# Kernel tuning notes

Hardware: AMD Instinct MI355X
Metric: run time of the kernel (lower is better)

## Reference

```python
import jax, jax.numpy as jnp
import numpy as np

D_MODEL = 1024
N_HEADS = 16
D_K = 64
D_FF = 4096
B = 8
S = 1024
NEG = -1e32
EPS = 1e-5


def _layer_norm(x, g, b):
    mu = jnp.mean(x, axis=-1, keepdims=True)
    var = jnp.var(x, axis=-1, keepdims=True)
    return (x - mu) * jax.lax.rsqrt(var + EPS) * g + b


def setup_inputs() -> dict:
    key = jax.random.key(0)
    ks = jax.random.split(key, 16)
    sc = 0.02
    inp = {
        'x': jax.random.normal(ks[0], (B, S, D_MODEL), dtype=jnp.float32),
        'Wq': jax.random.normal(ks[1], (D_MODEL, D_MODEL), jnp.float32) * sc,
        'bq': jnp.zeros((D_MODEL,), jnp.float32),
        'Wk': jax.random.normal(ks[2], (D_MODEL, D_MODEL), jnp.float32) * sc,
        'bk': jnp.zeros((D_MODEL,), jnp.float32),
        'Wv': jax.random.normal(ks[3], (D_MODEL, D_MODEL), jnp.float32) * sc,
        'bv': jnp.zeros((D_MODEL,), jnp.float32),
        'Wo': jax.random.normal(ks[4], (D_MODEL, D_MODEL), jnp.float32) * sc,
        'bo': jnp.zeros((D_MODEL,), jnp.float32),
        'W1': jax.random.normal(ks[5], (D_MODEL, D_FF), jnp.float32) * sc,
        'b1': jnp.zeros((D_FF,), jnp.float32),
        'W2': jax.random.normal(ks[6], (D_FF, D_MODEL), jnp.float32) * sc,
        'b2': jnp.zeros((D_MODEL,), jnp.float32),
        'g1': jnp.ones((D_MODEL,), jnp.float32),
        'beta1': jnp.zeros((D_MODEL,), jnp.float32),
        'g3': jnp.ones((D_MODEL,), jnp.float32),
        'beta3': jnp.zeros((D_MODEL,), jnp.float32),
    }
    return inp


def _block(x, Wq, bq, Wk, bk, Wv, bv, Wo, bo, W1, b1, W2, b2, g1, beta1, g3, beta3):
    bs, seqlen, _ = x.shape
    # QKV projections -> [b, h, s, d_k]
    def split_heads(t):
        return t.reshape(bs, seqlen, N_HEADS, D_K).transpose(0, 2, 1, 3)
    q = split_heads(x @ Wq + bq)
    k = split_heads(x @ Wk + bk)
    v = split_heads(x @ Wv + bv)
    # scores [b,h,s,s]
    scores = jnp.einsum('bhqd,bhkd->bhqk', q, k) / jnp.sqrt(jnp.float32(D_K))
    # mask=0 case: src_mask = (triu(ones, k=0) == 0) -> allow strictly lower (j < i)
    i = jnp.arange(seqlen)[:, None]
    j = jnp.arange(seqlen)[None, :]
    allowed = (j < i)  # [s, s]
    scores = jnp.where(allowed[None, None], scores, NEG)
    attn = jax.nn.softmax(scores, axis=-1)
    # zero_pad: zero out the first query row of attention probs
    attn = attn * (i > 0).astype(attn.dtype)[None, None]
    ctx = jnp.einsum('bhqk,bhkd->bhqd', attn, v)  # [b,h,s,d_k]
    concat = ctx.transpose(0, 2, 1, 3).reshape(bs, seqlen, D_MODEL)
    attn_out = concat @ Wo + bo
    # residual + LN (dropout p=0)
    h1 = _layer_norm(x + attn_out, g1, beta1)
    # position-wise FFN
    ffn = jax.nn.relu(h1 @ W1 + b1) @ W2 + b2
    out = _layer_norm(h1 + ffn, g3, beta3)
    return out


def reference(x, Wq, bq, Wk, bk, Wv, bv, Wo, bo, W1, b1, W2, b2, g1, beta1, g3, beta3):
    return _block(x, Wq, bq, Wk, bk, Wv, bv, Wo, bo, W1, b1, W2, b2, g1, beta1, g3, beta3)
```

## Files before the change

kernel.cpp:

```cpp
#include <hip/hip_runtime.h>
#include <hip/hip_bf16.h>

typedef __bf16 bf16x8 __attribute__((ext_vector_type(8)));
typedef __bf16 bf16x4 __attribute__((ext_vector_type(4)));
typedef float f32x4 __attribute__((ext_vector_type(4)));

#define GLOBAL_LOAD_LDS16(gp, lp)                                              \
  __builtin_amdgcn_global_load_lds(                                            \
      (const __attribute__((address_space(1))) void*)(gp),                     \
      (__attribute__((address_space(3))) void*)(lp), 16, 0, 0)

__global__ __launch_bounds__(256) void transpose4_f2b_k(
    const float* __restrict__ s0, const float* __restrict__ s1,
    const float* __restrict__ s2, const float* __restrict__ s3,
    __bf16* __restrict__ dst) {
  __shared__ float tile[32][33];
  const float* srcs[4] = {s0, s1, s2, s3};
  const float* src = srcs[blockIdx.z];
  __bf16* d = dst + ((size_t)blockIdx.z << 20);
  const int bx = blockIdx.x * 32, by = blockIdx.y * 32;
  const int tx = threadIdx.x & 31, ty = threadIdx.x >> 5;
#pragma unroll
  for (int i = 0; i < 32; i += 8)
    tile[ty + i][tx] = src[(size_t)(by + ty + i) * 1024 + bx + tx];
  __syncthreads();
#pragma unroll
  for (int i = 0; i < 32; i += 8)
    d[(size_t)(bx + ty + i) * 1024 + by + tx] = (__bf16)tile[tx][ty + i];
}

__global__ __launch_bounds__(256) void transpose_f2b_k(
    const float* __restrict__ src, __bf16* __restrict__ dst, int R, int C) {
  __shared__ float tile[32][33];
  const int bx = blockIdx.x * 32, by = blockIdx.y * 32;
  const int tx = threadIdx.x & 31, ty = threadIdx.x >> 5;
#pragma unroll
  for (int i = 0; i < 32; i += 8)
    tile[ty + i][tx] = src[(size_t)(by + ty + i) * C + bx + tx];
  __syncthreads();
#pragma unroll
  for (int i = 0; i < 32; i += 8)
    dst[(size_t)(bx + ty + i) * R + by + tx] = (__bf16)tile[tx][ty + i];
}

__global__ __launch_bounds__(256) void transpose_v_k(
    const __bf16* __restrict__ src, __bf16* __restrict__ dst) {
  __shared__ __bf16 tile[32][33];
  const int bh = blockIdx.z;
  const int s0 = blockIdx.x * 32, d0 = blockIdx.y * 32;
  const size_t base = (size_t)bh << 16;
  const int tx = threadIdx.x & 31, ty = threadIdx.x >> 5;
#pragma unroll
  for (int i = 0; i < 32; i += 8)
    tile[ty + i][tx] = src[base + (size_t)(s0 + ty + i) * 64 + d0 + tx];
  __syncthreads();
#pragma unroll
  for (int i = 0; i < 32; i += 8)
    dst[base + (size_t)(d0 + ty + i) * 1024 + s0 + tx] = tile[tx][ty + i];
}

__global__ __launch_bounds__(256) void convert_f2b_k(const float* __restrict__ s,
                                                     __bf16* __restrict__ d) {
  const size_t i = ((size_t)blockIdx.x * 256 + threadIdx.x) * 4;
  const float4 v = *(const float4*)(s + i);
  bf16x4 o;
  o[0] = (__bf16)v.x; o[1] = (__bf16)v.y; o[2] = (__bf16)v.z; o[3] = (__bf16)v.w;
  *(bf16x4*)(d + i) = o;
}

__global__ void concat3_k(const float* a, const float* b, const float* c,
                          float* o) {
  int i = blockIdx.x * 256 + threadIdx.x;
  if (i < 1024) o[i] = a[i];
  else if (i < 2048) o[i] = b[i - 1024];
  else if (i < 3072) o[i] = c[i - 2048];
}

#define STG(P, rowbase, Kld, kbase, DST)                                       \
  do {                                                                         \
    GLOBAL_LOAD_LDS16((P) + (size_t)((rowbase) + wave * 16 + srow) * (Kld) +   \
                          (kbase) + sch8,                                      \
                      (DST) + wave * 1024);                                    \
    GLOBAL_LOAD_LDS16((P) + (size_t)((rowbase) + wave * 16 + 8 + srow) *       \
                              (Kld) + (kbase) + sch8,                          \
                      (DST) + wave * 1024 + 512);                              \
  } while (0)

template <int EPI>
__global__ __launch_bounds__(512, 2) void gemm_k3(const __bf16* __restrict__ A,
                                                  const __bf16* __restrict__ Bt,
                                                  const float* __restrict__ bias,
                                                  __bf16* __restrict__ C,
                                                  int M, int N, int K) {
  __shared__ __align__(16) __bf16 Abuf[3][256 * 64];
  __shared__ __align__(16) __bf16 Bbuf[3][128 * 64];
  const int tid = threadIdx.x;
  const int wave = tid >> 6, lane = tid & 63;
  const int quad = lane >> 4, l15 = lane & 15;
  const int wm = wave >> 1, wn = wave & 1;

  const int nwg = gridDim.x;
  const int cpx = nwg >> 3;
  const int bid = blockIdx.x;
  const int wg = (bid & 7) * cpx + (bid >> 3);
  const int gy = N >> 7;
  const int tm = wg / gy, tn = wg - tm * gy;
  const int m0 = tm << 8, n0 = tn << 7;

  const int srow = lane >> 3;
  const int sch8 = ((lane & 7) ^ srow) * 8;
  const int aoff = (wm * 64 + l15) * 64;
  const int boff = (wn * 64 + l15) * 64;
  const int c0 = (quad ^ (l15 & 7)) * 8;

  bf16x8 af[4][2], bfr[4][2];
  f32x4 acc[4][4] = {};

  const int NT = K >> 6;

  const __bf16* a_c = Abuf[0];
  const __bf16* a_n = Abuf[1];
  const __bf16* a_f = Abuf[2];
  const __bf16* b_c = Bbuf[0];
  const __bf16* b_n = Bbuf[1];
  const __bf16* b_f = Bbuf[2];

  STG(A, m0, K, 0, (__bf16*)a_c);
  STG(A, m0 + 128, K, 0, (__bf16*)a_c + 128 * 64);
  STG(Bt, n0, K, 0, (__bf16*)b_c);
  STG(A, m0, K, 64, (__bf16*)a_n);
  STG(A, m0 + 128, K, 64, (__bf16*)a_n + 128 * 64);
  STG(Bt, n0, K, 64, (__bf16*)b_n);
  asm volatile("s_waitcnt vmcnt(6)" ::: "memory");
  __builtin_amdgcn_s_barrier();
  asm volatile("" ::: "memory");

  for (int t = 0; t < NT; ++t) {
#pragma unroll
    for (int f = 0; f < 4; ++f) {
      af[f][0] = *(const bf16x8*)(a_c + aoff + f * 1024 + c0);
      af[f][1] = *(const bf16x8*)(a_c + aoff + f * 1024 + (c0 ^ 32));
    }
#pragma unroll
    for (int g = 0; g < 4; ++g) {
      bfr[g][0] = *(const bf16x8*)(b_c + boff + g * 1024 + c0);
      bfr[g][1] = *(const bf16x8*)(b_c + boff + g * 1024 + (c0 ^ 32));
    }
    const int kf = (t + 2) << 6;
    const bool pf = (t + 2 < NT);
    if (pf) {
      STG(A, m0, K, kf, (__bf16*)a_f);
      STG(A, m0 + 128, K, kf, (__bf16*)a_f + 128 * 64);
      STG(Bt, n0, K, kf, (__bf16*)b_f);
    }
    __builtin_amdgcn_s_setprio(1);
#pragma unroll
    for (int f = 0; f < 4; ++f)
#pragma unroll
      for (int g = 0; g < 4; ++g) {
        acc[f][g] = __builtin_amdgcn_mfma_f32_16x16x32_bf16(
            af[f][0], bfr[g][0], acc[f][g], 0, 0, 0);
        acc[f][g] = __builtin_amdgcn_mfma_f32_16x16x32_bf16(
            af[f][1], bfr[g][1], acc[f][g], 0, 0, 0);
      }
    __builtin_amdgcn_s_setprio(0);
    if (pf) {
      asm volatile("s_waitcnt vmcnt(6)" ::: "memory");
      __builtin_amdgcn_s_barrier();
      asm volatile("" ::: "memory");
    } else if (t + 1 < NT) {
      asm volatile("s_waitcnt vmcnt(0)" ::: "memory");
      __builtin_amdgcn_s_barrier();
      asm volatile("" ::: "memory");
    }
    const __bf16* ta = a_c; a_c = a_n; a_n = a_f; a_f = ta;
    const __bf16* tb = b_c; b_c = b_n; b_n = b_f; b_f = tb;
  }

  float bvv[4];
#pragma unroll
  for (int g = 0; g < 4; ++g) bvv[g] = bias[n0 + wn * 64 + g * 16 + l15];
#pragma unroll
  for (int f = 0; f < 4; ++f)
#pragma unroll
    for (int i = 0; i < 4; ++i) {
      const int row = m0 + wm * 64 + f * 16 + quad * 4 + i;
#pragma unroll
      for (int g = 0; g < 4; ++g) {
        const int col = n0 + wn * 64 + g * 16 + l15;
        float v = acc[f][g][i] + bvv[g];
        if (EPI == 1) v = fmaxf(v, 0.0f);
        size_t oidx;
        if (EPI == 2) {
          const int which = col >> 10, wi = col & 1023;
          const int h = wi >> 6, d = wi & 63;
          const int b = row >> 10, s = row & 1023;
          oidx = ((size_t)which << 23) +
                 (((size_t)(b * 16 + h) << 16) + s * 64 + d);
        } else {
          oidx = (size_t)row * N + col;
        }
        C[oidx] = (__bf16)v;
      }
    }
}

__global__ __launch_bounds__(256) void attn_kernel(const __bf16* __restrict__ Q,
                                                   const __bf16* __restrict__ Kg,
                                                   const __bf16* __restrict__ Vt,
                                                   __bf16* __restrict__ ctx) {
  const int qp = blockIdx.x;
  const int bh = blockIdx.y;
  const int b = bh >> 4, h = bh & 15;
  const int tid = threadIdx.x, wave = tid >> 6, lane = tid & 63;
  const int quad = lane >> 4, l15 = lane & 15;
  const size_t hoff = (size_t)bh << 16;
  const __bf16* Qh = Q + hoff;
  const __bf16* Kh = Kg + hoff;
  const __bf16* Vh = Vt + hoff;

  __shared__ __align__(16) __bf16 Ks[64 * 64];
  __shared__ __align__(16) __bf16 Vs[64 * 64];
  __shared__ __align__(16) __bf16 Ps[4][32 * 72];
  __shared__ float lL[128];

  const int skey = wave * 8 + (lane >> 3);
  const int sgr = lane & 7;

#pragma unroll
  for (int pass = 0; pass < 2; ++pass) {
    const int qt = pass ? (7 - qp) : qp;
    const int qb = qt * 128;

    bf16x8 qf[2][2];
#pragma unroll
    for (int g = 0; g < 2; ++g) {
      const int qrow = qb + wave * 32 + g * 16 + l15;
      bf16x8 t0 = *(const bf16x8*)(Qh + (size_t)qrow * 64 + quad * 8);
      bf16x8 t1 = *(const bf16x8*)(Qh + (size_t)qrow * 64 + 32 + quad * 8);
#pragma unroll
      for (int e = 0; e < 8; ++e) {
        qf[g][0][e] = (__bf16)((float)t0[e] * 0.125f);
        qf[g][1][e] = (__bf16)((float)t1[e] * 0.125f);
      }
    }

    f32x4 oacc[4][2] = {};
    float lrun[2][4] = {};

    const int ktmax = 2 * qt + 1;
    for (int kt = 0; kt <= ktmax; ++kt) {
      __syncthreads();
#pragma unroll
      for (int j = 0; j < 2; ++j) {
        const int row = skey + 32 * j;
        GLOBAL_LOAD_LDS16(
            Kh + (size_t)(kt * 64 + row) * 64 + ((sgr ^ (row & 7)) * 8),
            Ks + j * 2048 + wave * 512);
        GLOBAL_LOAD_LDS16(
            Vh + (size_t)row * 1024 + kt * 64 + ((sgr ^ (row & 7)) * 8),
            Vs + j * 2048 + wave * 512);
      }
      __syncthreads();

      f32x4 sacc[2][4] = {};
#pragma unroll
      for (int nt = 0; nt < 4; ++nt) {
        const int key = nt * 16 + l15, sw = key & 7;
        bf16x8 kf0 = *(const bf16x8*)(Ks + key * 64 + ((quad ^ sw) * 8));
        bf16x8 kf1 = *(const bf16x8*)(Ks + key * 64 + (((quad + 4) ^ sw) * 8));
#pragma unroll
        for (int g = 0; g < 2; ++g) {
          sacc[g][nt] = __builtin_amdgcn_mfma_f32_16x16x32_bf16(
              qf[g][0], kf0, sacc[g][nt], 0, 0, 0);
          sacc[g][nt] = __builtin_amdgcn_mfma_f32_16x16x32_bf16(
              qf[g][1], kf1, sacc[g][nt], 0, 0, 0);
        }
      }

      const bool tilemask = (kt >= 2 * qt);
#pragma unroll
      for (int g = 0; g < 2; ++g)
#pragma unroll
        for (int nt = 0; nt < 4; ++nt) {
          const int key = kt * 64 + nt * 16 + l15;
#pragma unroll
          for (int r = 0; r < 4; ++r) {
            float p = __expf(fminf(sacc[g][nt][r], 60.0f));
            if (tilemask && key >= qb + wave * 32 + g * 16 + quad * 4 + r)
              p = 0.0f;
            sacc[g][nt][r] = p;
            lrun[g][r] += p;
          }
        }

#pragma unroll
      for (int g = 0; g < 2; ++g)
#pragma unroll
        for (int nt = 0; nt < 4; ++nt)
#pragma unroll
          for (int r = 0; r < 4; ++r)
            Ps[wave][(g * 16 + quad * 4 + r) * 72 + nt * 16 + l15] =
                (__bf16)sacc[g][nt][r];

#pragma unroll
      for (int kc = 0; kc < 2; ++kc) {
        bf16x8 pf[2];
#pragma unroll
        for (int g = 0; g < 2; ++g)
          pf[g] = *(const bf16x8*)(&Ps[wave][(g * 16 + l15) * 72 + kc * 32 +
                                             quad * 8]);
#pragma unroll
        for (int mdt = 0; mdt < 4; ++mdt) {
          const int d = mdt * 16 + l15, sw = d & 7;
          bf16x8 vf =
              *(const bf16x8*)(Vs + d * 64 + (((kc * 4 + quad) ^ sw) * 8));
#pragma unroll
          for (int g = 0; g < 2; ++g)
            oacc[mdt][g] = __builtin_amdgcn_mfma_f32_16x16x32_bf16(
                vf, pf[g], oacc[mdt][g], 0, 0, 0);
        }
      }
    }

#pragma unroll
    for (int g = 0; g < 2; ++g)
#pragma unroll
      for (int r = 0; r < 4; ++r) {
        float s = lrun[g][r];
#pragma unroll
        for (int d = 1; d < 16; d <<= 1) s += __shfl_xor(s, d);
        if (l15 == 0) lL[wave * 32 + g * 16 + quad * 4 + r] = s;
      }
    float linv[2];
#pragma unroll
    for (int g = 0; g < 2; ++g) {
      const float l = lL[wave * 32 + g * 16 + l15];
      linv[g] = (qb + wave * 32 + g * 16 + l15 == 0) ? 0.0f : (1.0f / l);
    }
    __bf16* Ot = Ps[wave];
#pragma unroll
    for (int mdt = 0; mdt < 4; ++mdt)
#pragma unroll
      for (int g = 0; g < 2; ++g)
#pragma unroll
        for (int r = 0; r < 4; ++r)
          Ot[(g * 16 + l15) * 72 + mdt * 16 + quad * 4 + r] =
              (__bf16)(oacc[mdt][g][r] * linv[g]);
#pragma unroll
    for (int rr = 0; rr < 2; ++rr)
#pragma unroll
      for (int j = 0; j < 2; ++j) {
        const int row = rr * 16 + (lane >> 2), chk = (lane & 3) + 4 * j;
        bf16x8 ov = *(const bf16x8*)(Ot + row * 72 + chk * 8);
        const size_t oi = ((size_t)(b * 1024 + qb + wave * 32 + row)) * 1024 +
                          h * 64 + chk * 8;
        *(bf16x8*)(ctx + oi) = ov;
      }
  }
}

template <typename TX, typename TY, typename TO>
__global__ __launch_bounds__(256) void add_ln_kernel(const TX* __restrict__ x,
                                                     const TY* __restrict__ y,
                                                     const float* __restrict__ g,
                                                     const float* __restrict__ be,
                                                     TO* __restrict__ out) {
  const int row = blockIdx.x;
  const size_t base = (size_t)row * 1024;
  const int t = threadIdx.x;
  float xv[4], yv[4];
  if constexpr (sizeof(TX) == 4) {
    const float4 a = *(const float4*)(x + base + t * 4);
    xv[0] = a.x; xv[1] = a.y; xv[2] = a.z; xv[3] = a.w;
  } else {
    const bf16x4 a = *(const bf16x4*)(x + base + t * 4);
#pragma unroll
    for (int i = 0; i < 4; ++i) xv[i] = (float)a[i];
  }
  if constexpr (sizeof(TY) == 4) {
    const float4 a = *(const float4*)(y + base + t * 4);
    yv[0] = a.x; yv[1] = a.y; yv[2] = a.z; yv[3] = a.w;
  } else {
    const bf16x4 a = *(const bf16x4*)(y + base + t * 4);
#pragma unroll
    for (int i = 0; i < 4; ++i) yv[i] = (float)a[i];
  }
  float v[4], s = 0.0f, s2 = 0.0f;
#pragma unroll
  for (int i = 0; i < 4; ++i) {
    v[i] = xv[i] + yv[i];
    s += v[i];
    s2 += v[i] * v[i];
  }
#pragma unroll
  for (int m = 1; m < 64; m <<= 1) {
    s += __shfl_xor(s, m);
    s2 += __shfl_xor(s2, m);
  }
  __shared__ float ss[4], ss2[4];
  const int w = t >> 6;
  if ((t & 63) == 0) { ss[w] = s; ss2[w] = s2; }
  __syncthreads();
  s = ss[0] + ss[1] + ss[2] + ss[3];
  s2 = ss2[0] + ss2[1] + ss2[2] + ss2[3];
  const float mu = s * (1.0f / 1024.0f);
  const float var = s2 * (1.0f / 1024.0f) - mu * mu;
  const float rstd = rsqrtf(var + 1e-5f);
#pragma unroll
  for (int i = 0; i < 4; ++i) {
    const float o = (v[i] - mu) * rstd * g[t * 4 + i] + be[t * 4 + i];
    out[base + t * 4 + i] = (TO)o;
  }
}

extern "C" void kernel_launch(void* const* d_in, const int* in_sizes, int n_in,
                              void* d_out, int out_size, void* d_ws,
                              size_t ws_size, hipStream_t stream) {
  (void)in_sizes; (void)n_in; (void)out_size; (void)ws_size;
  const float* x   = (const float*)d_in[0];
  const float* Wq  = (const float*)d_in[1];
  const float* bq  = (const float*)d_in[2];
  const float* Wk  = (const float*)d_in[3];
  const float* bk  = (const float*)d_in[4];
  const float* Wv  = (const float*)d_in[5];
  const float* bv  = (const float*)d_in[6];
  const float* Wo  = (const float*)d_in[7];
  const float* bo  = (const float*)d_in[8];
  const float* W1  = (const float*)d_in[9];
  const float* b1  = (const float*)d_in[10];
  const float* W2  = (const float*)d_in[11];
  const float* b2  = (const float*)d_in[12];
  const float* g1  = (const float*)d_in[13];
  const float* be1 = (const float*)d_in[14];
  const float* g3  = (const float*)d_in[15];
  const float* be3 = (const float*)d_in[16];

  char* ws = (char*)d_ws;
  __bf16* Qb    = (__bf16*)(ws + 0);
  __bf16* Kb    = (__bf16*)(ws + (16u << 20));
  __bf16* Vb    = (__bf16*)(ws + (32u << 20));
  __bf16* ctx   = (__bf16*)(ws + (48u << 20));
  __bf16* mid   = (__bf16*)(ws + 0);
  __bf16* aout  = (__bf16*)(ws + (64u << 20));
  __bf16* h1    = aout;
  __bf16* xb    = (__bf16*)(ws + (80u << 20));
  __bf16* Vtb   = (__bf16*)(ws + (80u << 20));
  __bf16* fout  = (__bf16*)(ws + (80u << 20));
  __bf16* WqkvT = (__bf16*)(ws + (96u << 20));
  __bf16* WoT   = (__bf16*)(ws + (96u << 20) + 3 * (1u << 21));
  __bf16* W1T   = (__bf16*)(ws + (104u << 20));
  __bf16* W2T   = (__bf16*)(ws + (112u << 20));
  float*  bqkv  = (float*)(ws + (120u << 20));
  float*  outp  = (float*)d_out;

  const dim3 blk(256);
  const dim3 blk512(512);
  convert_f2b_k<<<dim3(8192), blk, 0, stream>>>(x, xb);
  transpose4_f2b_k<<<dim3(32, 32, 4), blk, 0, stream>>>(Wq, Wk, Wv, Wo, WqkvT);
  transpose_f2b_k<<<dim3(128, 32), blk, 0, stream>>>(W1, W1T, 1024, 4096);
  transpose_f2b_k<<<dim3(32, 128), blk, 0, stream>>>(W2, W2T, 4096, 1024);
  concat3_k<<<dim3(12), blk, 0, stream>>>(bq, bk, bv, bqkv);

  gemm_k3<2><<<dim3(32 * 24), blk512, 0, stream>>>(xb, WqkvT, bqkv, Qb,
                                                   8192, 3072, 1024);
  transpose_v_k<<<dim3(32, 2, 128), blk, 0, stream>>>(Vb, Vtb);
  attn_kernel<<<dim3(4, 128), blk, 0, stream>>>(Qb, Kb, Vtb, ctx);
  gemm_k3<0><<<dim3(32 * 8), blk512, 0, stream>>>(ctx, WoT, bo, aout,
                                                  8192, 1024, 1024);
  add_ln_kernel<float, __bf16, __bf16><<<dim3(8192), blk, 0, stream>>>(
      x, aout, g1, be1, h1);
  gemm_k3<1><<<dim3(32 * 32), blk512, 0, stream>>>(h1, W1T, b1, mid,
                                                   8192, 4096, 1024);
  gemm_k3<0><<<dim3(32 * 8), blk512, 0, stream>>>(mid, W2T, b2, fout,
                                                  8192, 1024, 4096);
  add_ln_kernel<__bf16, __bf16, float><<<dim3(8192), blk, 0, stream>>>(
      h1, fout, g3, be3, outp);
}
```

Measured before the change: 471.2 us.

## Replace triple-buffered 256x128 GEMM with double-buffered 128x128 tile kernel

The GEMM tile shrinks from 256x128 with 512 threads to 128x128 with 256 threads (4 waves), and the LDS pipeline drops from three buffers to two with a one-stage prefetch. The grids double to match. This cuts LDS use and register pressure per block so more blocks can be resident, and gives more blocks for load balance. The cost is less data reuse per tile and a shallower prefetch that waits on vmcnt(0) every iteration, exposing more global-load latency.

```diff
diff --git a/kernel.cpp b/kernel.cpp
--- a/kernel.cpp
+++ b/kernel.cpp
@@ -87,13 +87,13 @@
   } while (0)
 
 template <int EPI>
-__global__ __launch_bounds__(512, 2) void gemm_k3(const __bf16* __restrict__ A,
+__global__ __launch_bounds__(256, 2) void gemm_db(const __bf16* __restrict__ A,
                                                   const __bf16* __restrict__ Bt,
                                                   const float* __restrict__ bias,
                                                   __bf16* __restrict__ C,
                                                   int M, int N, int K) {
-  __shared__ __align__(16) __bf16 Abuf[3][256 * 64];
-  __shared__ __align__(16) __bf16 Bbuf[3][128 * 64];
+  __shared__ __align__(16) __bf16 Abuf[2][128 * 64];
+  __shared__ __align__(16) __bf16 Bbuf[2][128 * 64];
   const int tid = threadIdx.x;
   const int wave = tid >> 6, lane = tid & 63;
   const int quad = lane >> 4, l15 = lane & 15;
@@ -105,7 +105,7 @@
   const int wg = (bid & 7) * cpx + (bid >> 3);
   const int gy = N >> 7;
   const int tm = wg / gy, tn = wg - tm * gy;
-  const int m0 = tm << 8, n0 = tn << 7;
+  const int m0 = tm << 7, n0 = tn << 7;
 
   const int srow = lane >> 3;
   const int sch8 = ((lane & 7) ^ srow) * 8;
@@ -120,18 +120,14 @@
 
   const __bf16* a_c = Abuf[0];
   const __bf16* a_n = Abuf[1];
-  const __bf16* a_f = Abuf[2];
   const __bf16* b_c = Bbuf[0];
   const __bf16* b_n = Bbuf[1];
-  const __bf16* b_f = Bbuf[2];
 
   STG(A, m0, K, 0, (__bf16*)a_c);
-  STG(A, m0 + 128, K, 0, (__bf16*)a_c + 128 * 64);
+  STG(A, m0 + 64, K, 0, (__bf16*)a_c + 64 * 64);
   STG(Bt, n0, K, 0, (__bf16*)b_c);
-  STG(A, m0, K, 64, (__bf16*)a_n);
-  STG(A, m0 + 128, K, 64, (__bf16*)a_n + 128 * 64);
-  STG(Bt, n0, K, 64, (__bf16*)b_n);
-  asm volatile("s_waitcnt vmcnt(6)" ::: "memory");
+  STG(Bt, n0 + 64, K, 0, (__bf16*)b_c + 64 * 64);
+  asm volatile("s_waitcnt vmcnt(0)" ::: "memory");
   __builtin_amdgcn_s_barrier();
   asm volatile("" ::: "memory");
 
@@ -146,12 +142,13 @@
       bfr[g][0] = *(const bf16x8*)(b_c + boff + g * 1024 + c0);
       bfr[g][1] = *(const bf16x8*)(b_c + boff + g * 1024 + (c0 ^ 32));
     }
-    const int kf = (t + 2) << 6;
-    const bool pf = (t + 2 < NT);
+    const int kn = (t + 1) << 6;
+    const bool pf = (t + 1 < NT);
     if (pf) {
-      STG(A, m0, K, kf, (__bf16*)a_f);
-      STG(A, m0 + 128, K, kf, (__bf16*)a_f + 128 * 64);
-      STG(Bt, n0, K, kf, (__bf16*)b_f);
+      STG(A, m0, K, kn, (__bf16*)a_n);
+      STG(A, m0 + 64, K, kn, (__bf16*)a_n + 64 * 64);
+      STG(Bt, n0, K, kn, (__bf16*)b_n);
+      STG(Bt, n0 + 64, K, kn, (__bf16*)b_n + 64 * 64);
     }
     __builtin_amdgcn_s_setprio(1);
 #pragma unroll
@@ -165,16 +162,12 @@
       }
     __builtin_amdgcn_s_setprio(0);
     if (pf) {
-      asm volatile("s_waitcnt vmcnt(6)" ::: "memory");
-      __builtin_amdgcn_s_barrier();
-      asm volatile("" ::: "memory");
-    } else if (t + 1 < NT) {
       asm volatile("s_waitcnt vmcnt(0)" ::: "memory");
       __builtin_amdgcn_s_barrier();
       asm volatile("" ::: "memory");
     }
-    const __bf16* ta = a_c; a_c = a_n; a_n = a_f; a_f = ta;
-    const __bf16* tb = b_c; b_c = b_n; b_n = b_f; b_f = tb;
+    const __bf16* ta = a_c; a_c = a_n; a_n = ta;
+    const __bf16* tb = b_c; b_c = b_n; b_n = tb;
   }
 
   float bvv[4];
@@ -455,25 +448,24 @@
   float*  outp  = (float*)d_out;
 
   const dim3 blk(256);
-  const dim3 blk512(512);
   convert_f2b_k<<<dim3(8192), blk, 0, stream>>>(x, xb);
   transpose4_f2b_k<<<dim3(32, 32, 4), blk, 0, stream>>>(Wq, Wk, Wv, Wo, WqkvT);
   transpose_f2b_k<<<dim3(128, 32), blk, 0, stream>>>(W1, W1T, 1024, 4096);
   transpose_f2b_k<<<dim3(32, 128), blk, 0, stream>>>(W2, W2T, 4096, 1024);
   concat3_k<<<dim3(12), blk, 0, stream>>>(bq, bk, bv, bqkv);
 
-  gemm_k3<2><<<dim3(32 * 24), blk512, 0, stream>>>(xb, WqkvT, bqkv, Qb,
-                                                   8192, 3072, 1024);
+  gemm_db<2><<<dim3(64 * 24), blk, 0, stream>>>(xb, WqkvT, bqkv, Qb,
+                                                8192, 3072, 1024);
   transpose_v_k<<<dim3(32, 2, 128), blk, 0, stream>>>(Vb, Vtb);
   attn_kernel<<<dim3(4, 128), blk, 0, stream>>>(Qb, Kb, Vtb, ctx);
-  gemm_k3<0><<<dim3(32 * 8), blk512, 0, stream>>>(ctx, WoT, bo, aout,
-                                                  8192, 1024, 1024);
+  gemm_db<0><<<dim3(64 * 8), blk, 0, stream>>>(ctx, WoT, bo, aout,
+                                               8192, 1024, 1024);
   add_ln_kernel<float, __bf16, __bf16><<<dim3(8192), blk, 0, stream>>>(
       x, aout, g1, be1, h1);
-  gemm_k3<1><<<dim3(32 * 32), blk512, 0, stream>>>(h1, W1T, b1, mid,
-                                                   8192, 4096, 1024);
-  gemm_k3<0><<<dim3(32 * 8), blk512, 0, stream>>>(mid, W2T, b2, fout,
-                                                  8192, 1024, 4096);
+  gemm_db<1><<<dim3(64 * 32), blk, 0, stream>>>(h1, W1T, b1, mid,
+                                                8192, 4096, 1024);
+  gemm_db<0><<<dim3(64 * 8), blk, 0, stream>>>(mid, W2T, b2, fout,
+                                               8192, 1024, 4096);
   add_ln_kernel<__bf16, __bf16, float><<<dim3(8192), blk, 0, stream>>>(
       h1, fout, g3, be3, outp);
 }
```

New measurement: 461.5 us. -2.1%, faster.

## Rewrite GEMM as 256-thread kernel with K=32 stages, templated M tile, grouped tile order

Applied to the files above, without the earlier changes.

Replaces the 512-thread 256x128x64 GEMM with a 256-thread kernel that uses K-steps of 32 and a templated M tile (256 or 128). The smaller N=1024 GEMMs switch to 128-row tiles to raise block count. Workgroups are remapped into 8x8 super-tiles to improve L2 reuse, and the LDS swizzle is adjusted to the narrower rows. Each wave now carries a larger accumulator tile and gets twice as many barrier iterations per K, which may add synchronisation overhead and register pressure.

```diff
diff --git a/kernel.cpp b/kernel.cpp
--- a/kernel.cpp
+++ b/kernel.cpp
@@ -76,24 +76,21 @@
   else if (i < 3072) o[i] = c[i - 2048];
 }
 
-#define STG(P, rowbase, Kld, kbase, DST)                                       \
-  do {                                                                         \
-    GLOBAL_LOAD_LDS16((P) + (size_t)((rowbase) + wave * 16 + srow) * (Kld) +   \
-                          (kbase) + sch8,                                      \
-                      (DST) + wave * 1024);                                    \
-    GLOBAL_LOAD_LDS16((P) + (size_t)((rowbase) + wave * 16 + 8 + srow) *       \
-                              (Kld) + (kbase) + sch8,                          \
-                      (DST) + wave * 1024 + 512);                              \
-  } while (0)
-
-template <int EPI>
-__global__ __launch_bounds__(512, 2) void gemm_k3(const __bf16* __restrict__ A,
+#define STG32(P, rowbase, Kld, kbase, DST)                                     \
+  GLOBAL_LOAD_LDS16((P) + (size_t)((rowbase) + (lane >> 2)) * (Kld) +          \
+                        (kbase) + s32,                                         \
+                    (DST))
+
+template <int EPI, int BM>
+__global__ __launch_bounds__(256, 2) void gemm_t3(const __bf16* __restrict__ A,
                                                   const __bf16* __restrict__ Bt,
                                                   const float* __restrict__ bias,
                                                   __bf16* __restrict__ C,
                                                   int M, int N, int K) {
-  __shared__ __align__(16) __bf16 Abuf[3][256 * 64];
-  __shared__ __align__(16) __bf16 Bbuf[3][128 * 64];
+  constexpr int F = BM / 32;
+  constexpr int LA = BM / 64;
+  __shared__ __align__(16) __bf16 Abuf[3][BM * 32];
+  __shared__ __align__(16) __bf16 Bbuf[3][128 * 32];
   const int tid = threadIdx.x;
   const int wave = tid >> 6, lane = tid & 63;
   const int quad = lane >> 4, l15 = lane & 15;
@@ -104,19 +101,23 @@
   const int bid = blockIdx.x;
   const int wg = (bid & 7) * cpx + (bid >> 3);
   const int gy = N >> 7;
-  const int tm = wg / gy, tn = wg - tm * gy;
-  const int m0 = tm << 8, n0 = tn << 7;
-
-  const int srow = lane >> 3;
-  const int sch8 = ((lane & 7) ^ srow) * 8;
-  const int aoff = (wm * 64 + l15) * 64;
-  const int boff = (wn * 64 + l15) * 64;
-  const int c0 = (quad ^ (l15 & 7)) * 8;
-
-  bf16x8 af[4][2], bfr[4][2];
-  f32x4 acc[4][4] = {};
-
-  const int NT = K >> 6;
+  const int nstc = gy >> 3;
+  const int st = wg >> 6;
+  const int r = wg & 63;
+  const int stm = st / nstc, stn = st - stm * nstc;
+  const int tm = (stm << 3) + (r >> 3);
+  const int tn = (stn << 3) + (r & 7);
+  const int m0 = tm * BM, n0 = tn << 7;
+
+  const int s32 = (((lane & 3) ^ ((lane >> 3) & 3)) * 8);
+  const int c0 = (quad ^ ((l15 >> 1) & 3)) * 8;
+  const int aoff = (wm * (BM / 2) + l15) * 32;
+  const int boff = (wn * 64 + l15) * 32;
+
+  bf16x8 af[F], bfr[4];
+  f32x4 acc[F][4] = {};
+
+  const int NT = K >> 5;
 
   const __bf16* a_c = Abuf[0];
   const __bf16* a_n = Abuf[1];
@@ -125,47 +126,49 @@
   const __bf16* b_n = Bbuf[1];
   const __bf16* b_f = Bbuf[2];
 
-  STG(A, m0, K, 0, (__bf16*)a_c);
-  STG(A, m0 + 128, K, 0, (__bf16*)a_c + 128 * 64);
-  STG(Bt, n0, K, 0, (__bf16*)b_c);
-  STG(A, m0, K, 64, (__bf16*)a_n);
-  STG(A, m0 + 128, K, 64, (__bf16*)a_n + 128 * 64);
-  STG(Bt, n0, K, 64, (__bf16*)b_n);
-  asm volatile("s_waitcnt vmcnt(6)" ::: "memory");
+#define STAGE_TILE(kb, AD, BD)                                                 \
+  do {                                                                         \
+    _Pragma("unroll") for (int p_ = 0; p_ < LA; ++p_)                          \
+        STG32(A, m0 + wave * (BM / 4) + p_ * 16, K, kb,                        \
+              (__bf16*)(AD) + (wave * (BM / 4) + p_ * 16) * 32);               \
+    _Pragma("unroll") for (int p_ = 0; p_ < 2; ++p_)                           \
+        STG32(Bt, n0 + wave * 32 + p_ * 16, K, kb,                             \
+              (__bf16*)(BD) + (wave * 32 + p_ * 16) * 32);                     \
+  } while (0)
+
+#define WAIT_L()                                                               \
+  do {                                                                         \
+    if constexpr (BM == 256)                                                   \
+      asm volatile("s_waitcnt vmcnt(6)" ::: "memory");                         \
+    else                                                                       \
+      asm volatile("s_waitcnt vmcnt(4)" ::: "memory");                         \
+  } while (0)
+
+  STAGE_TILE(0, a_c, b_c);
+  STAGE_TILE(32, a_n, b_n);
+  WAIT_L();
   __builtin_amdgcn_s_barrier();
   asm volatile("" ::: "memory");
 
   for (int t = 0; t < NT; ++t) {
 #pragma unroll
-    for (int f = 0; f < 4; ++f) {
-      af[f][0] = *(const bf16x8*)(a_c + aoff + f * 1024 + c0);
-      af[f][1] = *(const bf16x8*)(a_c + aoff + f * 1024 + (c0 ^ 32));
-    }
-#pragma unroll
-    for (int g = 0; g < 4; ++g) {
-      bfr[g][0] = *(const bf16x8*)(b_c + boff + g * 1024 + c0);
-      bfr[g][1] = *(const bf16x8*)(b_c + boff + g * 1024 + (c0 ^ 32));
-    }
-    const int kf = (t + 2) << 6;
+    for (int f = 0; f < F; ++f)
+      af[f] = *(const bf16x8*)(a_c + aoff + f * 512 + c0);
+#pragma unroll
+    for (int g = 0; g < 4; ++g)
+      bfr[g] = *(const bf16x8*)(b_c + boff + g * 512 + c0);
     const bool pf = (t + 2 < NT);
-    if (pf) {
-      STG(A, m0, K, kf, (__bf16*)a_f);
-      STG(A, m0 + 128, K, kf, (__bf16*)a_f + 128 * 64);
-      STG(Bt, n0, K, kf, (__bf16*)b_f);
-    }
+    if (pf) STAGE_TILE((t + 2) << 5, a_f, b_f);
     __builtin_amdgcn_s_setprio(1);
 #pragma unroll
-    for (int f = 0; f < 4; ++f)
-#pragma unroll
-      for (int g = 0; g < 4; ++g) {
+    for (int f = 0; f < F; ++f)
+#pragma unroll
+      for (int g = 0; g < 4; ++g)
         acc[f][g] = __builtin_amdgcn_mfma_f32_16x16x32_bf16(
-            af[f][0], bfr[g][0], acc[f][g], 0, 0, 0);
-        acc[f][g] = __builtin_amdgcn_mfma_f32_16x16x32_bf16(
-            af[f][1], bfr[g][1], acc[f][g], 0, 0, 0);
-      }
+            af[f], bfr[g], acc[f][g], 0, 0, 0);
     __builtin_amdgcn_s_setprio(0);
     if (pf) {
-      asm volatile("s_waitcnt vmcnt(6)" ::: "memory");
+      WAIT_L();
       __builtin_amdgcn_s_barrier();
       asm volatile("" ::: "memory");
     } else if (t + 1 < NT) {
@@ -181,10 +184,10 @@
 #pragma unroll
   for (int g = 0; g < 4; ++g) bvv[g] = bias[n0 + wn * 64 + g * 16 + l15];
 #pragma unroll
-  for (int f = 0; f < 4; ++f)
+  for (int f = 0; f < F; ++f)
 #pragma unroll
     for (int i = 0; i < 4; ++i) {
-      const int row = m0 + wm * 64 + f * 16 + quad * 4 + i;
+      const int row = m0 + wm * (BM / 2) + f * 16 + quad * 4 + i;
 #pragma unroll
       for (int g = 0; g < 4; ++g) {
         const int col = n0 + wn * 64 + g * 16 + l15;
@@ -203,6 +206,8 @@
         C[oidx] = (__bf16)v;
       }
     }
+#undef STAGE_TILE
+#undef WAIT_L
 }
 
 __global__ __launch_bounds__(256) void attn_kernel(const __bf16* __restrict__ Q,
@@ -455,25 +460,24 @@
   float*  outp  = (float*)d_out;
 
   const dim3 blk(256);
-  const dim3 blk512(512);
   convert_f2b_k<<<dim3(8192), blk, 0, stream>>>(x, xb);
   transpose4_f2b_k<<<dim3(32, 32, 4), blk, 0, stream>>>(Wq, Wk, Wv, Wo, WqkvT);
   transpose_f2b_k<<<dim3(128, 32), blk, 0, stream>>>(W1, W1T, 1024, 4096);
   transpose_f2b_k<<<dim3(32, 128), blk, 0, stream>>>(W2, W2T, 4096, 1024);
   concat3_k<<<dim3(12), blk, 0, stream>>>(bq, bk, bv, bqkv);
 
-  gemm_k3<2><<<dim3(32 * 24), blk512, 0, stream>>>(xb, WqkvT, bqkv, Qb,
-                                                   8192, 3072, 1024);
+  gemm_t3<2, 256><<<dim3(768), blk, 0, stream>>>(xb, WqkvT, bqkv, Qb,
+                                                 8192, 3072, 1024);
   transpose_v_k<<<dim3(32, 2, 128), blk, 0, stream>>>(Vb, Vtb);
   attn_kernel<<<dim3(4, 128), blk, 0, stream>>>(Qb, Kb, Vtb, ctx);
-  gemm_k3<0><<<dim3(32 * 8), blk512, 0, stream>>>(ctx, WoT, bo, aout,
-                                                  8192, 1024, 1024);
+  gemm_t3<0, 128><<<dim3(512), blk, 0, stream>>>(ctx, WoT, bo, aout,
+                                                 8192, 1024, 1024);
   add_ln_kernel<float, __bf16, __bf16><<<dim3(8192), blk, 0, stream>>>(
       x, aout, g1, be1, h1);
-  gemm_k3<1><<<dim3(32 * 32), blk512, 0, stream>>>(h1, W1T, b1, mid,
-                                                   8192, 4096, 1024);
-  gemm_k3<0><<<dim3(32 * 8), blk512, 0, stream>>>(mid, W2T, b2, fout,
-                                                  8192, 1024, 4096);
+  gemm_t3<1, 256><<<dim3(1024), blk, 0, stream>>>(h1, W1T, b1, mid,
+                                                  8192, 4096, 1024);
+  gemm_t3<0, 128><<<dim3(512), blk, 0, stream>>>(mid, W2T, b2, fout,
+                                                 8192, 1024, 4096);
   add_ln_kernel<__bf16, __bf16, float><<<dim3(8192), blk, 0, stream>>>(
       h1, fout, g3, be3, outp);
 }
```

Measured after the change: 485.7 us. 3.1% more time.
